# Optimization experiments

Measured on AMD Instinct MI355X. Metric: run time of the kernel, lower is better.

The kernel has to match this reference:

```python
import jax, jax.numpy as jnp
import numpy as np

NUM_USERS = 50000
NUM_ITEMS = 50000
N_NODES = NUM_USERS + NUM_ITEMS
EMBED_DIM = 64
NUM_LAYERS = 2
NUM_EDGES = 3200000


def setup_inputs() -> dict:
    key = jax.random.key(0)
    ks = jax.random.split(key, 8)
    edge_index = jax.random.randint(ks[0], (2, NUM_EDGES), 0, N_NODES, dtype=jnp.int32)
    edge_weight = jax.random.uniform(ks[1], (NUM_EDGES,), dtype=jnp.float32)
    scale = 1.0 / np.sqrt(EMBED_DIM)
    user_emb = jax.random.normal(ks[2], (NUM_USERS, EMBED_DIM), dtype=jnp.float32)
    item_emb = jax.random.normal(ks[3], (NUM_ITEMS, EMBED_DIM), dtype=jnp.float32)
    W1 = jax.random.normal(ks[4], (EMBED_DIM, EMBED_DIM), dtype=jnp.float32) * scale
    b1 = jnp.zeros((EMBED_DIM,), dtype=jnp.float32)
    W2 = jax.random.normal(ks[5], (EMBED_DIM, EMBED_DIM), dtype=jnp.float32) * scale
    b2 = jnp.zeros((EMBED_DIM,), dtype=jnp.float32)
    return {"edge_index": edge_index, "edge_weight": edge_weight,
            "user_emb": user_emb, "item_emb": item_emb,
            "W1": W1, "b1": b1, "W2": W2, "b2": b2}


def _gcn_layer(x, edge_index, edge_weight, W, b):
    # message: x_j * w_e ; aggregate: scatter-add to target nodes
    src, dst = edge_index[0], edge_index[1]
    msgs = x[src] * edge_weight[:, None]              # [E, D]
    agg = jax.ops.segment_sum(msgs, dst, num_segments=N_NODES)  # [N, D]
    updated = (agg + x) * 0.5                          # residual average
    return updated @ W.T + b                           # nn.Linear


def reference(edge_index, edge_weight, user_emb, item_emb, W1, b1, W2, b2):
    x = jnp.concatenate([user_emb, item_emb], axis=0)  # [N, D]
    x = _gcn_layer(x, edge_index, edge_weight, W1, b1)
    x = _gcn_layer(x, edge_index, edge_weight, W2, b2)
    return x
```

## Files before the change

kernel.cpp:

```cpp
#include <hip/hip_runtime.h>

#define N_NODES 100000
#define NUM_U 50000
#define D 64
#define NUM_E 3200000
#define NB 391
#define PBLK 500
#define CHUNK (NUM_E / PBLK)
#define CHUNK4 (CHUNK / 4)
#define FCAP 8928

__device__ __forceinline__ float bf2f(unsigned short u) {
  return __uint_as_float((unsigned)u << 16);
}
__device__ __forceinline__ unsigned short f2bf(float f) {
  unsigned u = __float_as_uint(f);
  u += 0x7FFF + ((u >> 16) & 1);
  return (unsigned short)(u >> 16);
}

__global__ __launch_bounds__(256) void micro_kernel(
    const float* __restrict__ W1, const float* __restrict__ W2,
    const float* __restrict__ b1, const float* __restrict__ b2,
    float* __restrict__ M, float* __restrict__ c, float* __restrict__ cc) {
  __shared__ float w1[64][65], w2[64][65];
  int t = (int)threadIdx.x;
  for (int i = t; i < 4096; i += 256) { w1[i >> 6][i & 63] = W1[i]; w2[i >> 6][i & 63] = W2[i]; }
  __syncthreads();
  for (int i = t; i < 4096; i += 256) {
    int k = i >> 6, j = i & 63;
    float s = 0.f;
#pragma unroll
    for (int tt = 0; tt < 64; ++tt) s = fmaf(w2[j][tt], w1[tt][k], s);
    M[i] = s;
  }
  if (t < 64) {
    float s = 0.f;
#pragma unroll
    for (int tt = 0; tt < 64; ++tt) s = fmaf(b1[tt], w2[t][tt], s);
    c[t] = s;
    cc[t] = 0.5f * s + b2[t];
  }
}

__global__ __launch_bounds__(256) void zmm_kernel(
    const float* __restrict__ xu, const float* __restrict__ xi,
    const float* __restrict__ M, unsigned short* __restrict__ z16) {
  __shared__ float Mt[64][65];
  __shared__ float U[64][65];
  int t = (int)threadIdx.x;
  for (int i = t; i < 4096; i += 256) Mt[i & 63][i >> 6] = M[i];
  int lane = t & 63, row = t >> 6;
  int n0 = (int)blockIdx.x * 64;
#pragma unroll
  for (int i = 0; i < 16; ++i) {
    int nl = row + 4 * i, n = n0 + nl;
    if (n < N_NODES) {
      const float* xr = (n < NUM_U) ? (xu + (size_t)n * D) : (xi + (size_t)(n - NUM_U) * D);
      U[nl][lane] = xr[lane];
    }
  }
  __syncthreads();
#pragma unroll
  for (int i = 0; i < 16; ++i) {
    int nl = row + 4 * i, n = n0 + nl;
    if (n >= N_NODES) continue;
    float s = 0.f;
#pragma unroll
    for (int k = 0; k < 64; ++k) s = fmaf(U[nl][k], Mt[lane][k], s);
    z16[(size_t)n * D + lane] = f2bf(s);
  }
}

__global__ __launch_bounds__(256) void p1_hist(const int4* __restrict__ dst4,
                                               int* __restrict__ tot) {
  __shared__ int h[NB];
  int t = (int)threadIdx.x, blk = (int)blockIdx.x;
  for (int i = t; i < NB; i += 256) h[i] = 0;
  __syncthreads();
  int base4 = blk * CHUNK4;
  for (int i = t; i < CHUNK4; i += 256) {
    int4 d = dst4[base4 + i];
    atomicAdd(&h[d.x >> 8], 1); atomicAdd(&h[d.y >> 8], 1);
    atomicAdd(&h[d.z >> 8], 1); atomicAdd(&h[d.w >> 8], 1);
  }
  __syncthreads();
  for (int i = t; i < NB; i += 256)
    if (h[i]) atomicAdd(&tot[i], h[i]);
}

__global__ __launch_bounds__(512) void p2_scan(const int* __restrict__ tot,
                                               int* __restrict__ bbase,
                                               int* __restrict__ gcursor,
                                               int* __restrict__ rowptr) {
  __shared__ int ps[512];
  int t = (int)threadIdx.x;
  int v = (t < NB) ? tot[t] : 0;
  ps[t] = v;
  __syncthreads();
  for (int o = 1; o < 512; o <<= 1) {
    int a = (t >= o) ? ps[t - o] : 0;
    __syncthreads();
    ps[t] += a;
    __syncthreads();
  }
  if (t < NB) { int e = ps[t] - v; bbase[t] = e; gcursor[t] = e; }
  if (t == 0) { bbase[NB] = NUM_E; rowptr[N_NODES] = NUM_E; }
}

__global__ __launch_bounds__(512) void p3_part(const int4* __restrict__ src4,
                                               const int4* __restrict__ dst4,
                                               const float4* __restrict__ w4,
                                               int* __restrict__ gcursor,
                                               int2* __restrict__ staging) {
  __shared__ int2 ent[CHUNK];
  __shared__ int h[NB];
  __shared__ int lst[NB + 1];
  __shared__ int og[NB];
  __shared__ int ps[512];
  int t = (int)threadIdx.x, blk = (int)blockIdx.x;
  for (int i = t; i < NB; i += 512) h[i] = 0;
  __syncthreads();
  int base4 = blk * CHUNK4;
  for (int i = t; i < CHUNK4; i += 512) {
    int4 d = dst4[base4 + i];
    atomicAdd(&h[d.x >> 8], 1); atomicAdd(&h[d.y >> 8], 1);
    atomicAdd(&h[d.z >> 8], 1); atomicAdd(&h[d.w >> 8], 1);
  }
  __syncthreads();
  int v = (t < NB) ? h[t] : 0;
  ps[t] = v;
  __syncthreads();
  for (int o = 1; o < 512; o <<= 1) {
    int a = (t >= o) ? ps[t - o] : 0;
    __syncthreads();
    ps[t] += a;
    __syncthreads();
  }
  if (t < NB) {
    lst[t] = ps[t] - v;
    og[t] = v ? atomicAdd(&gcursor[t], v) : 0;
  }
  if (t == 0) lst[NB] = CHUNK;
  __syncthreads();
  if (t < NB) h[t] = lst[t];
  __syncthreads();
  for (int i = t; i < CHUNK4; i += 512) {
    int4 s = src4[base4 + i];
    int4 d = dst4[base4 + i];
    float4 w = w4[base4 + i];
    int p;
    p = atomicAdd(&h[d.x >> 8], 1);
    ent[p] = make_int2(s.x | ((d.x & 255) << 17), __float_as_int(w.x));
    p = atomicAdd(&h[d.y >> 8], 1);
    ent[p] = make_int2(s.y | ((d.y & 255) << 17), __float_as_int(w.y));
    p = atomicAdd(&h[d.z >> 8], 1);
    ent[p] = make_int2(s.z | ((d.z & 255) << 17), __float_as_int(w.z));
    p = atomicAdd(&h[d.w >> 8], 1);
    ent[p] = make_int2(s.w | ((d.w & 255) << 17), __float_as_int(w.w));
  }
  __syncthreads();
  for (int i = t; i < CHUNK; i += 512) {
    int lo = 0, hi = NB;
    while (hi - lo > 1) { int mid = (lo + hi) >> 1; if (lst[mid] <= i) lo = mid; else hi = mid; }
    staging[og[lo] + (i - lst[lo])] = ent[i];
  }
}

__global__ __launch_bounds__(256) void csr_finalize(
    const int* __restrict__ bbase, const int2* __restrict__ staging,
    int2* __restrict__ meta, int* __restrict__ rowptr) {
  __shared__ int2 ent[FCAP];
  __shared__ int hist[256], ps[256], cur[256];
  int t = (int)threadIdx.x, b = (int)blockIdx.x;
  int bs = bbase[b], be = bbase[b + 1];
  int cnt = be - bs;
  hist[t] = 0;
  __syncthreads();
  for (int i = bs + t; i < be; i += 256) atomicAdd(&hist[staging[i].x >> 17], 1);
  __syncthreads();
  int v = hist[t];
  ps[t] = v;
  __syncthreads();
  for (int o = 1; o < 256; o <<= 1) {
    int a = (t >= o) ? ps[t - o] : 0;
    __syncthreads();
    ps[t] += a;
    __syncthreads();
  }
  int lexcl = ps[t] - v;
  int n = b * 256 + t;
  if (n < N_NODES) rowptr[n] = bs + lexcl;
  if (cnt <= FCAP) {
    cur[t] = lexcl;
    __syncthreads();
    for (int i = bs + t; i < be; i += 256) {
      int2 m = staging[i];
      int p = atomicAdd(&cur[m.x >> 17], 1);
      ent[p] = make_int2(m.x & 0x1FFFF, m.y);
    }
    __syncthreads();
    for (int i = t; i < cnt; i += 256) meta[bs + i] = ent[i];
  } else {
    cur[t] = bs + lexcl;
    __syncthreads();
    for (int i = bs + t; i < be; i += 256) {
      int2 m = staging[i];
      int p = atomicAdd(&cur[m.x >> 17], 1);
      meta[p] = make_int2(m.x & 0x1FFFF, m.y);
    }
  }
}

template <bool FINAL>
__global__ __launch_bounds__(256) void gather_kernel(
    const int* __restrict__ rowptr, const int2* __restrict__ meta,
    const unsigned short* __restrict__ gsrc, const unsigned short* __restrict__ z16,
    const float* __restrict__ c, const float* __restrict__ cc,
    float* __restrict__ outf, unsigned short* __restrict__ out16) {
  int t = (int)threadIdx.x, lane = t & 63;
  int wid = (int)((blockIdx.x * blockDim.x + t) >> 6);
  int nw = (int)((gridDim.x * blockDim.x) >> 6);
  float cl = FINAL ? c[lane] : 0.f;
  float ccl = FINAL ? cc[lane] : 0.f;

  for (int n = wid; n < N_NODES; n += nw) {
    int lo = __builtin_amdgcn_readfirstlane(rowptr[n]);
    int hi = __builtin_amdgcn_readfirstlane(rowptr[n + 1]);
    float acc0 = 0.f, acc1 = 0.f, wsum = 0.f;
    int j = lo;
    for (; j + 16 <= hi; j += 16) {
      int2 mm[16];
      float vv[16];
#pragma unroll
      for (int q = 0; q < 16; ++q) mm[q] = meta[j + q];
#pragma unroll
      for (int q = 0; q < 16; ++q) vv[q] = bf2f(gsrc[((size_t)mm[q].x << 6) + lane]);
#pragma unroll
      for (int q = 0; q < 16; ++q) {
        if (q & 1) acc1 = fmaf(vv[q], __int_as_float(mm[q].y), acc1);
        else       acc0 = fmaf(vv[q], __int_as_float(mm[q].y), acc0);
      }
      if (FINAL) {
        float s0 = 0.f, s1 = 0.f;
#pragma unroll
        for (int q = 0; q < 16; q += 2) {
          s0 += __int_as_float(mm[q].y);
          s1 += __int_as_float(mm[q + 1].y);
        }
        wsum += s0 + s1;
      }
    }
    for (; j + 4 <= hi; j += 4) {
      int2 m0 = meta[j + 0], m1 = meta[j + 1], m2 = meta[j + 2], m3 = meta[j + 3];
      float v0 = bf2f(gsrc[((size_t)m0.x << 6) + lane]);
      float v1 = bf2f(gsrc[((size_t)m1.x << 6) + lane]);
      float v2 = bf2f(gsrc[((size_t)m2.x << 6) + lane]);
      float v3 = bf2f(gsrc[((size_t)m3.x << 6) + lane]);
      acc0 = fmaf(v0, __int_as_float(m0.y), acc0);
      acc1 = fmaf(v1, __int_as_float(m1.y), acc1);
      acc0 = fmaf(v2, __int_as_float(m2.y), acc0);
      acc1 = fmaf(v3, __int_as_float(m3.y), acc1);
      if (FINAL)
        wsum += (__int_as_float(m0.y) + __int_as_float(m1.y)) +
                (__int_as_float(m2.y) + __int_as_float(m3.y));
    }
    for (; j < hi; ++j) {
      int2 m = meta[j];
      acc0 = fmaf(bf2f(gsrc[((size_t)m.x << 6) + lane]), __int_as_float(m.y), acc0);
      if (FINAL) wsum += __int_as_float(m.y);
    }
    float acc = acc0 + acc1;
    size_t o = ((size_t)n << 6) + lane;
    if (FINAL) {
      float t1n = bf2f(gsrc[o]);
      float zn = bf2f(z16[o]);
      outf[o] = 0.25f * acc + 0.5f * t1n + 0.25f * zn + 0.5f * wsum * cl + ccl;
    } else {
      out16[o] = f2bf(acc);
    }
  }
}

extern "C" void kernel_launch(void* const* d_in, const int* in_sizes, int n_in,
                              void* d_out, int out_size, void* d_ws, size_t ws_size,
                              hipStream_t stream) {
  const int* edge_index = (const int*)d_in[0];
  const int* src = edge_index;
  const int* dst = edge_index + NUM_E;
  const float* w = (const float*)d_in[1];
  const float* user_emb = (const float*)d_in[2];
  const float* item_emb = (const float*)d_in[3];
  const float* W1 = (const float*)d_in[4];
  const float* b1 = (const float*)d_in[5];
  const float* W2 = (const float*)d_in[6];
  const float* b2 = (const float*)d_in[7];
  float* out = (float*)d_out;

  unsigned short* z16 = (unsigned short*)d_ws;
  int2* staging = (int2*)(z16 + (size_t)N_NODES * D);
  unsigned short* t1_16 = (unsigned short*)staging;
  int2* meta = staging + NUM_E;
  int* rowptr = (int*)(meta + NUM_E);
  int* tot = rowptr + 100352;
  int* bbase = tot + 392;
  int* gcursor = bbase + 392;
  float* Mbuf = (float*)(gcursor + 392);
  float* cbuf = Mbuf + 4096;
  float* ccbuf = cbuf + 64;

  hipMemsetAsync(tot, 0, NB * sizeof(int), stream);

  micro_kernel<<<1, 256, 0, stream>>>(W1, W2, b1, b2, Mbuf, cbuf, ccbuf);
  zmm_kernel<<<(N_NODES + 63) / 64, 256, 0, stream>>>(user_emb, item_emb, Mbuf, z16);

  p1_hist<<<PBLK, 256, 0, stream>>>((const int4*)dst, tot);
  p2_scan<<<1, 512, 0, stream>>>(tot, bbase, gcursor, rowptr);
  p3_part<<<PBLK, 512, 0, stream>>>((const int4*)src, (const int4*)dst,
                                    (const float4*)w, gcursor, staging);
  csr_finalize<<<NB, 256, 0, stream>>>(bbase, staging, meta, rowptr);

  gather_kernel<false><<<2048, 256, 0, stream>>>(rowptr, meta, z16, z16, cbuf,
                                                 ccbuf, nullptr, t1_16);
  gather_kernel<true><<<2048, 256, 0, stream>>>(rowptr, meta, t1_16, z16, cbuf,
                                                ccbuf, out, nullptr);
}
```

Measured before the change: 413.7 us.

## Fuse CSR build stages into one cooperative kernel and shrink gather unroll

Replaces the memset plus the histogram, scan, partition and finalize kernels with a single cooperative kernel that separates the phases with grid-wide syncs. This removes several launch boundaries and the separate memset. In exchange it adds grid barrier costs and a larger shared-memory footprint per block. Separately, the gather loop's main unroll drops from 16 to 8 edges, which cuts register pressure but leaves fewer loads in flight per wave.

```diff
diff --git a/kernel.cpp b/kernel.cpp
--- a/kernel.cpp
+++ b/kernel.cpp
@@ -1,4 +1,7 @@
 #include <hip/hip_runtime.h>
+#include <hip/hip_cooperative_groups.h>
+
+namespace cg = cooperative_groups;
 
 #define N_NODES 100000
 #define NUM_U 50000
@@ -6,6 +9,7 @@
 #define NUM_E 3200000
 #define NB 391
 #define PBLK 500
+#define BT 512
 #define CHUNK (NUM_E / PBLK)
 #define CHUNK4 (CHUNK / 4)
 #define FCAP 8928
@@ -72,142 +76,146 @@
   }
 }
 
-__global__ __launch_bounds__(256) void p1_hist(const int4* __restrict__ dst4,
-                                               int* __restrict__ tot) {
-  __shared__ int h[NB];
+__global__ __launch_bounds__(BT) void build_kernel(
+    const int4* __restrict__ src4, const int4* __restrict__ dst4,
+    const float4* __restrict__ w4, int* __restrict__ tot,
+    int* __restrict__ bbase, int* __restrict__ gcursor,
+    int* __restrict__ rowptr, int2* __restrict__ staging,
+    int2* __restrict__ meta) {
+  __shared__ int2 ent[FCAP];
+  __shared__ int sA[BT], sB[BT], sC[BT], sD[BT];
+  cg::grid_group grid = cg::this_grid();
   int t = (int)threadIdx.x, blk = (int)blockIdx.x;
-  for (int i = t; i < NB; i += 256) h[i] = 0;
-  __syncthreads();
-  int base4 = blk * CHUNK4;
-  for (int i = t; i < CHUNK4; i += 256) {
-    int4 d = dst4[base4 + i];
-    atomicAdd(&h[d.x >> 8], 1); atomicAdd(&h[d.y >> 8], 1);
-    atomicAdd(&h[d.z >> 8], 1); atomicAdd(&h[d.w >> 8], 1);
-  }
-  __syncthreads();
-  for (int i = t; i < NB; i += 256)
-    if (h[i]) atomicAdd(&tot[i], h[i]);
-}
-
-__global__ __launch_bounds__(512) void p2_scan(const int* __restrict__ tot,
-                                               int* __restrict__ bbase,
-                                               int* __restrict__ gcursor,
-                                               int* __restrict__ rowptr) {
-  __shared__ int ps[512];
-  int t = (int)threadIdx.x;
-  int v = (t < NB) ? tot[t] : 0;
-  ps[t] = v;
-  __syncthreads();
-  for (int o = 1; o < 512; o <<= 1) {
-    int a = (t >= o) ? ps[t - o] : 0;
-    __syncthreads();
-    ps[t] += a;
-    __syncthreads();
-  }
-  if (t < NB) { int e = ps[t] - v; bbase[t] = e; gcursor[t] = e; }
-  if (t == 0) { bbase[NB] = NUM_E; rowptr[N_NODES] = NUM_E; }
-}
-
-__global__ __launch_bounds__(512) void p3_part(const int4* __restrict__ src4,
-                                               const int4* __restrict__ dst4,
-                                               const float4* __restrict__ w4,
-                                               int* __restrict__ gcursor,
-                                               int2* __restrict__ staging) {
-  __shared__ int2 ent[CHUNK];
-  __shared__ int h[NB];
-  __shared__ int lst[NB + 1];
-  __shared__ int og[NB];
-  __shared__ int ps[512];
-  int t = (int)threadIdx.x, blk = (int)blockIdx.x;
-  for (int i = t; i < NB; i += 512) h[i] = 0;
-  __syncthreads();
-  int base4 = blk * CHUNK4;
-  for (int i = t; i < CHUNK4; i += 512) {
-    int4 d = dst4[base4 + i];
-    atomicAdd(&h[d.x >> 8], 1); atomicAdd(&h[d.y >> 8], 1);
-    atomicAdd(&h[d.z >> 8], 1); atomicAdd(&h[d.w >> 8], 1);
-  }
-  __syncthreads();
-  int v = (t < NB) ? h[t] : 0;
-  ps[t] = v;
-  __syncthreads();
-  for (int o = 1; o < 512; o <<= 1) {
-    int a = (t >= o) ? ps[t - o] : 0;
-    __syncthreads();
-    ps[t] += a;
-    __syncthreads();
-  }
-  if (t < NB) {
-    lst[t] = ps[t] - v;
-    og[t] = v ? atomicAdd(&gcursor[t], v) : 0;
-  }
-  if (t == 0) lst[NB] = CHUNK;
-  __syncthreads();
-  if (t < NB) h[t] = lst[t];
-  __syncthreads();
-  for (int i = t; i < CHUNK4; i += 512) {
-    int4 s = src4[base4 + i];
-    int4 d = dst4[base4 + i];
-    float4 w = w4[base4 + i];
-    int p;
-    p = atomicAdd(&h[d.x >> 8], 1);
-    ent[p] = make_int2(s.x | ((d.x & 255) << 17), __float_as_int(w.x));
-    p = atomicAdd(&h[d.y >> 8], 1);
-    ent[p] = make_int2(s.y | ((d.y & 255) << 17), __float_as_int(w.y));
-    p = atomicAdd(&h[d.z >> 8], 1);
-    ent[p] = make_int2(s.z | ((d.z & 255) << 17), __float_as_int(w.z));
-    p = atomicAdd(&h[d.w >> 8], 1);
-    ent[p] = make_int2(s.w | ((d.w & 255) << 17), __float_as_int(w.w));
-  }
-  __syncthreads();
-  for (int i = t; i < CHUNK; i += 512) {
-    int lo = 0, hi = NB;
-    while (hi - lo > 1) { int mid = (lo + hi) >> 1; if (lst[mid] <= i) lo = mid; else hi = mid; }
-    staging[og[lo] + (i - lst[lo])] = ent[i];
-  }
-}
-
-__global__ __launch_bounds__(256) void csr_finalize(
-    const int* __restrict__ bbase, const int2* __restrict__ staging,
-    int2* __restrict__ meta, int* __restrict__ rowptr) {
-  __shared__ int2 ent[FCAP];
-  __shared__ int hist[256], ps[256], cur[256];
-  int t = (int)threadIdx.x, b = (int)blockIdx.x;
-  int bs = bbase[b], be = bbase[b + 1];
-  int cnt = be - bs;
-  hist[t] = 0;
-  __syncthreads();
-  for (int i = bs + t; i < be; i += 256) atomicAdd(&hist[staging[i].x >> 17], 1);
-  __syncthreads();
-  int v = hist[t];
-  ps[t] = v;
-  __syncthreads();
-  for (int o = 1; o < 256; o <<= 1) {
-    int a = (t >= o) ? ps[t - o] : 0;
-    __syncthreads();
-    ps[t] += a;
-    __syncthreads();
-  }
-  int lexcl = ps[t] - v;
-  int n = b * 256 + t;
-  if (n < N_NODES) rowptr[n] = bs + lexcl;
-  if (cnt <= FCAP) {
-    cur[t] = lexcl;
-    __syncthreads();
-    for (int i = bs + t; i < be; i += 256) {
-      int2 m = staging[i];
-      int p = atomicAdd(&cur[m.x >> 17], 1);
-      ent[p] = make_int2(m.x & 0x1FFFF, m.y);
-    }
-    __syncthreads();
-    for (int i = t; i < cnt; i += 256) meta[bs + i] = ent[i];
-  } else {
-    cur[t] = bs + lexcl;
-    __syncthreads();
-    for (int i = bs + t; i < be; i += 256) {
-      int2 m = staging[i];
-      int p = atomicAdd(&cur[m.x >> 17], 1);
-      meta[p] = make_int2(m.x & 0x1FFFF, m.y);
+
+  for (int i = t; i < NB; i += BT) tot[i] = 0;
+  grid.sync();
+
+  {
+    int* h = sA;
+    for (int i = t; i < NB; i += BT) h[i] = 0;
+    __syncthreads();
+    int base4 = blk * CHUNK4;
+    for (int i = t; i < CHUNK4; i += BT) {
+      int4 d = dst4[base4 + i];
+      atomicAdd(&h[d.x >> 8], 1); atomicAdd(&h[d.y >> 8], 1);
+      atomicAdd(&h[d.z >> 8], 1); atomicAdd(&h[d.w >> 8], 1);
+    }
+    __syncthreads();
+    for (int i = t; i < NB; i += BT)
+      if (h[i]) atomicAdd(&tot[i], h[i]);
+  }
+  grid.sync();
+
+  if (blk == 0) {
+    int* ps = sB;
+    int v = (t < NB) ? tot[t] : 0;
+    ps[t] = v;
+    __syncthreads();
+    for (int o = 1; o < BT; o <<= 1) {
+      int a = (t >= o) ? ps[t - o] : 0;
+      __syncthreads();
+      ps[t] += a;
+      __syncthreads();
+    }
+    if (t < NB) { int e = ps[t] - v; bbase[t] = e; gcursor[t] = e; }
+    if (t == 0) { bbase[NB] = NUM_E; rowptr[N_NODES] = NUM_E; }
+  }
+  grid.sync();
+
+  {
+    int* h = sA;
+    int* ps = sB;
+    int* lst = sC;
+    int* og = sD;
+    for (int i = t; i < NB; i += BT) h[i] = 0;
+    __syncthreads();
+    int base4 = blk * CHUNK4;
+    for (int i = t; i < CHUNK4; i += BT) {
+      int4 d = dst4[base4 + i];
+      atomicAdd(&h[d.x >> 8], 1); atomicAdd(&h[d.y >> 8], 1);
+      atomicAdd(&h[d.z >> 8], 1); atomicAdd(&h[d.w >> 8], 1);
+    }
+    __syncthreads();
+    int v = (t < NB) ? h[t] : 0;
+    ps[t] = v;
+    __syncthreads();
+    for (int o = 1; o < BT; o <<= 1) {
+      int a = (t >= o) ? ps[t - o] : 0;
+      __syncthreads();
+      ps[t] += a;
+      __syncthreads();
+    }
+    if (t < NB) {
+      lst[t] = ps[t] - v;
+      og[t] = v ? atomicAdd(&gcursor[t], v) : 0;
+    }
+    if (t == NB) lst[NB] = CHUNK;
+    __syncthreads();
+    if (t < NB) h[t] = lst[t];
+    __syncthreads();
+    for (int i = t; i < CHUNK4; i += BT) {
+      int4 s = src4[base4 + i];
+      int4 d = dst4[base4 + i];
+      float4 w = w4[base4 + i];
+      int p;
+      p = atomicAdd(&h[d.x >> 8], 1);
+      ent[p] = make_int2(s.x | ((d.x & 255) << 17), __float_as_int(w.x));
+      p = atomicAdd(&h[d.y >> 8], 1);
+      ent[p] = make_int2(s.y | ((d.y & 255) << 17), __float_as_int(w.y));
+      p = atomicAdd(&h[d.z >> 8], 1);
+      ent[p] = make_int2(s.z | ((d.z & 255) << 17), __float_as_int(w.z));
+      p = atomicAdd(&h[d.w >> 8], 1);
+      ent[p] = make_int2(s.w | ((d.w & 255) << 17), __float_as_int(w.w));
+    }
+    __syncthreads();
+    for (int i = t; i < CHUNK; i += BT) {
+      int lo = 0, hi = NB;
+      while (hi - lo > 1) { int mid = (lo + hi) >> 1; if (lst[mid] <= i) lo = mid; else hi = mid; }
+      staging[og[lo] + (i - lst[lo])] = ent[i];
+    }
+  }
+  grid.sync();
+
+  if (blk < NB) {
+    int* hist = sA;
+    int* ps = sB;
+    int* cur = sC;
+    int bs = bbase[blk], be = bbase[blk + 1];
+    int cnt = be - bs;
+    if (t < 256) hist[t] = 0;
+    __syncthreads();
+    for (int i = bs + t; i < be; i += BT) atomicAdd(&hist[staging[i].x >> 17], 1);
+    __syncthreads();
+    int v = (t < 256) ? hist[t] : 0;
+    if (t < 256) ps[t] = v;
+    __syncthreads();
+    for (int o = 1; o < 256; o <<= 1) {
+      int a = (t >= o && t < 256) ? ps[t - o] : 0;
+      __syncthreads();
+      if (t < 256) ps[t] += a;
+      __syncthreads();
+    }
+    int lexcl = (t < 256) ? (ps[t] - v) : 0;
+    int n = blk * 256 + t;
+    if (t < 256 && n < N_NODES) rowptr[n] = bs + lexcl;
+    if (cnt <= FCAP) {
+      if (t < 256) cur[t] = lexcl;
+      __syncthreads();
+      for (int i = bs + t; i < be; i += BT) {
+        int2 m = staging[i];
+        int p = atomicAdd(&cur[m.x >> 17], 1);
+        ent[p] = make_int2(m.x & 0x1FFFF, m.y);
+      }
+      __syncthreads();
+      for (int i = t; i < cnt; i += BT) meta[bs + i] = ent[i];
+    } else {
+      if (t < 256) cur[t] = bs + lexcl;
+      __syncthreads();
+      for (int i = bs + t; i < be; i += BT) {
+        int2 m = staging[i];
+        int p = atomicAdd(&cur[m.x >> 17], 1);
+        meta[p] = make_int2(m.x & 0x1FFFF, m.y);
+      }
     }
   }
 }
@@ -229,41 +237,32 @@
     int hi = __builtin_amdgcn_readfirstlane(rowptr[n + 1]);
     float acc0 = 0.f, acc1 = 0.f, wsum = 0.f;
     int j = lo;
-    for (; j + 16 <= hi; j += 16) {
-      int2 mm[16];
-      float vv[16];
-#pragma unroll
-      for (int q = 0; q < 16; ++q) mm[q] = meta[j + q];
-#pragma unroll
-      for (int q = 0; q < 16; ++q) vv[q] = bf2f(gsrc[((size_t)mm[q].x << 6) + lane]);
-#pragma unroll
-      for (int q = 0; q < 16; ++q) {
-        if (q & 1) acc1 = fmaf(vv[q], __int_as_float(mm[q].y), acc1);
-        else       acc0 = fmaf(vv[q], __int_as_float(mm[q].y), acc0);
-      }
-      if (FINAL) {
-        float s0 = 0.f, s1 = 0.f;
-#pragma unroll
-        for (int q = 0; q < 16; q += 2) {
-          s0 += __int_as_float(mm[q].y);
-          s1 += __int_as_float(mm[q + 1].y);
-        }
-        wsum += s0 + s1;
-      }
-    }
-    for (; j + 4 <= hi; j += 4) {
+    for (; j + 8 <= hi; j += 8) {
       int2 m0 = meta[j + 0], m1 = meta[j + 1], m2 = meta[j + 2], m3 = meta[j + 3];
+      int2 m4 = meta[j + 4], m5 = meta[j + 5], m6 = meta[j + 6], m7 = meta[j + 7];
       float v0 = bf2f(gsrc[((size_t)m0.x << 6) + lane]);
       float v1 = bf2f(gsrc[((size_t)m1.x << 6) + lane]);
       float v2 = bf2f(gsrc[((size_t)m2.x << 6) + lane]);
       float v3 = bf2f(gsrc[((size_t)m3.x << 6) + lane]);
+      float v4 = bf2f(gsrc[((size_t)m4.x << 6) + lane]);
+      float v5 = bf2f(gsrc[((size_t)m5.x << 6) + lane]);
+      float v6 = bf2f(gsrc[((size_t)m6.x << 6) + lane]);
+      float v7 = bf2f(gsrc[((size_t)m7.x << 6) + lane]);
       acc0 = fmaf(v0, __int_as_float(m0.y), acc0);
       acc1 = fmaf(v1, __int_as_float(m1.y), acc1);
       acc0 = fmaf(v2, __int_as_float(m2.y), acc0);
       acc1 = fmaf(v3, __int_as_float(m3.y), acc1);
-      if (FINAL)
-        wsum += (__int_as_float(m0.y) + __int_as_float(m1.y)) +
-                (__int_as_float(m2.y) + __int_as_float(m3.y));
+      acc0 = fmaf(v4, __int_as_float(m4.y), acc0);
+      acc1 = fmaf(v5, __int_as_float(m5.y), acc1);
+      acc0 = fmaf(v6, __int_as_float(m6.y), acc0);
+      acc1 = fmaf(v7, __int_as_float(m7.y), acc1);
+      if (FINAL) {
+        float wa = (__int_as_float(m0.y) + __int_as_float(m1.y)) +
+                   (__int_as_float(m2.y) + __int_as_float(m3.y));
+        float wb = (__int_as_float(m4.y) + __int_as_float(m5.y)) +
+                   (__int_as_float(m6.y) + __int_as_float(m7.y));
+        wsum += wa + wb;
+      }
     }
     for (; j < hi; ++j) {
       int2 m = meta[j];
@@ -286,8 +285,6 @@
                               void* d_out, int out_size, void* d_ws, size_t ws_size,
                               hipStream_t stream) {
   const int* edge_index = (const int*)d_in[0];
-  const int* src = edge_index;
-  const int* dst = edge_index + NUM_E;
   const float* w = (const float*)d_in[1];
   const float* user_emb = (const float*)d_in[2];
   const float* item_emb = (const float*)d_in[3];
@@ -309,16 +306,19 @@
   float* cbuf = Mbuf + 4096;
   float* ccbuf = cbuf + 64;
 
-  hipMemsetAsync(tot, 0, NB * sizeof(int), stream);
-
   micro_kernel<<<1, 256, 0, stream>>>(W1, W2, b1, b2, Mbuf, cbuf, ccbuf);
   zmm_kernel<<<(N_NODES + 63) / 64, 256, 0, stream>>>(user_emb, item_emb, Mbuf, z16);
 
-  p1_hist<<<PBLK, 256, 0, stream>>>((const int4*)dst, tot);
-  p2_scan<<<1, 512, 0, stream>>>(tot, bbase, gcursor, rowptr);
-  p3_part<<<PBLK, 512, 0, stream>>>((const int4*)src, (const int4*)dst,
-                                    (const float4*)w, gcursor, staging);
-  csr_finalize<<<NB, 256, 0, stream>>>(bbase, staging, meta, rowptr);
+  {
+    const int4* src4 = (const int4*)edge_index;
+    const int4* dst4 = (const int4*)(edge_index + NUM_E);
+    const float4* w4 = (const float4*)w;
+    void* args[] = {(void*)&src4, (void*)&dst4, (void*)&w4, (void*)&tot,
+                    (void*)&bbase, (void*)&gcursor, (void*)&rowptr,
+                    (void*)&staging, (void*)&meta};
+    hipLaunchCooperativeKernel((const void*)build_kernel, dim3(PBLK), dim3(BT),
+                               args, 0, stream);
+  }
 
   gather_kernel<false><<<2048, 256, 0, stream>>>(rowptr, meta, z16, z16, cbuf,
                                                  ccbuf, nullptr, t1_16);
```

After: 580.6 us. 1.4x slower.
